# Optimization experiments

Hardware: AMD Instinct MI355X
Metric: run time of the kernel (lower is better)

The kernel has to match this reference:

```python
import jax, jax.numpy as jnp
import numpy as np

N_NODES = 20000   # num_of_nodes + 1 (incl. prediction node)
FEAT = 256        # in_features == hidden_features == out_features
N_LAYERS = 2
ALPHA = 0.2       # LeakyReLU negative slope
V_OBS = 512       # observed codes per patient
D_H = np.sqrt(FEAT * 1.0)  # sqrt(hidden_features * num_of_heads), n_heads=1
EPS = 1e-6


def _fc_edges(nodes):
    # torch: source = nodes.repeat(1, n); dest = each node repeated n times
    n = len(nodes)
    return np.stack([np.tile(nodes, n), np.repeat(nodes, n)]).astype(np.int64)


def setup_inputs() -> dict:
    key = jax.random.key(0)
    ks = jax.random.split(key, 16)
    rng = np.random.default_rng(0)
    obs = np.sort(rng.choice(np.arange(1, N_NODES - 1), size=V_OBS, replace=False))
    input_edges = jnp.asarray(_fc_edges(obs))
    obs_out = np.concatenate([obs, [N_NODES - 1]])  # add prediction node
    output_edges = jnp.asarray(_fc_edges(obs_out))

    s = 0.02
    embed = s * jax.random.normal(ks[0], (N_NODES, FEAT), jnp.float32)
    embed = embed.at[0].set(0.0)  # padding_idx=0
    return {
        "embed": embed,
        "W_w": s * jax.random.normal(ks[1], (N_LAYERS, FEAT, FEAT), jnp.float32),
        "W_b": s * jax.random.normal(ks[2], (N_LAYERS, FEAT), jnp.float32),
        "a": s * jax.random.normal(ks[3], (N_LAYERS, 2 * FEAT), jnp.float32),
        "ln_a": jnp.ones((N_LAYERS, FEAT), jnp.float32),
        "ln_b": jnp.zeros((N_LAYERS, FEAT), jnp.float32),
        "Wo_w": s * jax.random.normal(ks[4], (FEAT, FEAT), jnp.float32),
        "Wo_b": s * jax.random.normal(ks[5], (FEAT,), jnp.float32),
        "ao": s * jax.random.normal(ks[6], (2 * FEAT,), jnp.float32),
        "lno_a": jnp.ones((FEAT,), jnp.float32),
        "lno_b": jnp.zeros((FEAT,), jnp.float32),
        "lin_w": s * jax.random.normal(ks[7], (FEAT, FEAT), jnp.float32),
        "lin_b": s * jax.random.normal(ks[8], (FEAT,), jnp.float32),
        "param_w": s * jax.random.normal(ks[9], (2 * FEAT, FEAT), jnp.float32),
        "param_b": s * jax.random.normal(ks[10], (2 * FEAT,), jnp.float32),
        "out1_w": s * jax.random.normal(ks[11], (FEAT, FEAT), jnp.float32),
        "out1_b": s * jax.random.normal(ks[12], (FEAT,), jnp.float32),
        "out2_w": s * jax.random.normal(ks[13], (1, FEAT), jnp.float32),
        "out2_b": s * jax.random.normal(ks[14], (1,), jnp.float32),
        "input_edges": input_edges,
        "output_edges": output_edges,
    }


def _attention(x, edges, Ww, Wb, avec):
    # d = Linear(x): (N, H)
    d = x @ Ww.T + Wb
    H = d.shape[1]
    # a . [d_src ; d_dst] == (d @ a_left)[src] + (d @ a_right)[dst]  (cheaper, same math)
    s_node = d @ avec[:H]
    t_node = d @ avec[H:]
    score = s_node[edges[0]] + t_node[edges[1]]                  # (E,)
    e = jnp.exp(jax.nn.leaky_relu(score, ALPHA) / D_H)           # unnormalized attn
    n = x.shape[0]
    rowsum = jax.ops.segment_sum(e, edges[0], num_segments=n)   # (N,)
    agg = jax.ops.segment_sum(e[:, None] * d[edges[1]], edges[0], num_segments=n)
    zero = rowsum == 0
    # rows with no in-edges get an identity self-edge of weight 1 and rowsum 1
    agg = agg + jnp.where(zero[:, None], d, 0.0)
    return agg / jnp.where(zero, 1.0, rowsum)[:, None]


def _layernorm(x, g, b):
    m = x.mean(-1, keepdims=True)
    s = jnp.std(x, axis=-1, ddof=1, keepdims=True)  # torch std: unbiased
    return g * (x - m) / (s + EPS) + b


def reference(embed, W_w, W_b, a, ln_a, ln_b, Wo_w, Wo_b, ao, lno_a, lno_b,
              lin_w, lin_b, param_w, param_b, out1_w, out1_b, out2_w, out2_b,
              input_edges, output_edges):
    h = embed  # embedding lookup of arange(N) == the full table
    for l in range(N_LAYERS):  # in_att stack, concat=True, n_heads=1: ffn = LN -> ELU
        h = jax.nn.elu(_layernorm(_attention(h, input_edges, W_w[l], W_b[l], a[l]),
                                  ln_a[l], ln_b[l]))
    # variational layer (eval mode: reparameterize returns mu)
    hp = (h @ param_w.T + param_b).reshape(-1, 2, FEAT)
    h = hp[:, 0, :]  # mu
    # out_att: concat=False, mean over 1 head; ffn = LN -> ReLU -> Linear
    g = _attention(h, output_edges, Wo_w, Wo_b, ao)
    g = jax.nn.relu(_layernorm(g, lno_a, lno_b)) @ lin_w.T + lin_b
    # out_layer on prediction node: ReLU -> Linear -> ReLU -> Linear(->1)
    z = jax.nn.relu(g[-1])
    z = jax.nn.relu(z @ out1_w.T + out1_b)
    logit = z @ out2_w.T + out2_b  # (1,)
    return logit
```

## Files before the change

kernel.cpp:

```cpp
#include <hip/hip_runtime.h>
#include <hip/hip_bf16.h>

#define FEAT 256
#define NOBS 512
#define NOUT 513
#define GAT_ALPHA 0.2f
#define INV_DH (1.0f / 16.0f)
#define LN_EPS 1e-6f


__device__ __forceinline__ float b2f(unsigned short u) {
    union { float f; unsigned v; } x;
    x.v = ((unsigned)u) << 16;
    return x.f;
}

__device__ __forceinline__ float loadv(const void* p, long idx, int isbf) {
    if (isbf) return b2f(((const unsigned short*)p)[idx]);
    return ((const float*)p)[idx];
}

__device__ __forceinline__ float4 load4(const void* p, long idx, int isbf) {
    if (isbf) {
        ushort4 u = *(const ushort4*)((const unsigned short*)p + idx);
        return make_float4(b2f(u.x), b2f(u.y), b2f(u.z), b2f(u.w));
    }
    return *(const float4*)((const float*)p + idx);
}

__device__ __forceinline__ int detect_bf(const void* w) {
    const unsigned short* hb = (const unsigned short*)w;
    int sane = 0;
#pragma unroll
    for (int i = 0; i < 32; i += 2) {
        float a = fabsf(b2f(hb[i]));
        sane += (a > 1e-4f && a < 0.3f) ? 1 : 0;
    }
    return (sane >= 8) ? 1 : 0;
}

__device__ __forceinline__ int detect_estep(const void* edges) {
    const int* ei = (const int*)edges;
    return (ei[1] == 0 && ei[3] == 0 && ei[5] == 0 && ei[7] == 0) ? 2 : 1;
}

__device__ __forceinline__ float wave_allreduce(float v) {
#pragma unroll
    for (int o = 1; o < 64; o <<= 1) v += __shfl_xor(v, o);
    return v;
}

__device__ __forceinline__ float bsum1024(float v, float* red) {
    __syncthreads();
    float s = wave_allreduce(v);
    int lane = threadIdx.x & 63, w = threadIdx.x >> 6;
    if (lane == 0) red[w] = s;
    __syncthreads();
    float t = 0.f;
#pragma unroll
    for (int i = 0; i < 16; i++) t += red[i];
    return t;
}

#define FV_AS0 0
#define FV_AS1 256
#define FV_AT0 512
#define FV_AT1 768
#define FV_WB0 1024
#define FV_WB1 1280
#define FV_LNA0 1536
#define FV_LNA1 1792
#define FV_LNB0 2048
#define FV_LNB1 2304
#define FV_WOB 2560
#define FV_AOS 2816
#define FV_AOT 3072
#define FV_LNOA 3328
#define FV_LNOB 3584
#define FV_LINB 3840
#define FV_PARB 4096
#define FV_O1B 4352
#define FV_O2W 4608
#define FV_O2B 4864

__global__ __launch_bounds__(256) void k_front(
        const void* embed, const void* W_w, const void* W_b, const void* a,
        const void* ln_a, const void* ln_b, const void* Wo_w, const void* Wo_b,
        const void* ao, const void* lno_a, const void* lno_b, const void* lin_w,
        const void* lin_b, const void* param_w, const void* param_b,
        const void* out1_w, const void* out1_b, const void* out2_w, const void* out2_b,
        const void* oedges, float* fv, float* packs,
        float* __restrict__ D1, float* S1, float* T1, int* done) {
    __shared__ __align__(16) char smem[37888];
    float (*xs)[FEAT] = (float(*)[FEAT])smem;
    float (*wl)[33] = (float(*)[33])(smem + 4096);
    float (*tile)[65] = (float(*)[65])smem;
    int isbf = detect_bf(W_w);
    int b = blockIdx.x, tid = threadIdx.x, lane = tid & 63, w = tid >> 6;
    if (b < 129) {
        int estep = detect_estep(oedges);
        int i0 = b << 2;
        int nr = NOUT - i0;
        if (nr > 4) nr = 4;
        if (w < nr) {
            const int* oe = (const int*)oedges;
            long node = oe[(long)(i0 + w) * estep];
            *(float4*)&xs[w][lane << 2] = load4(embed, node * FEAT + (lane << 2), isbf);
        } else {
#pragma unroll
            for (int q = 0; q < 4; q++) xs[w][(lane << 2) + q] = 0.f;
        }
        float acc[4] = {0.f, 0.f, 0.f, 0.f};
        int fb8 = tid >> 3;
        int kq = tid & 7;
        for (int kc = 0; kc < 8; kc++) {
            int k0 = kc << 5;
            __syncthreads();
#pragma unroll
            for (int i = 0; i < 8; i++) {
                int f = fb8 + (i << 5);
                float4 v = load4(W_w, (long)f * FEAT + k0 + (kq << 2), isbf);
                wl[f][(kq << 2) + 0] = v.x;
                wl[f][(kq << 2) + 1] = v.y;
                wl[f][(kq << 2) + 2] = v.z;
                wl[f][(kq << 2) + 3] = v.w;
            }
            __syncthreads();
#pragma unroll
            for (int k4 = 0; k4 < 8; k4++) {
                float4 x0 = ((const float4*)xs[0])[(kc << 3) + k4];
                float4 x1 = ((const float4*)xs[1])[(kc << 3) + k4];
                float4 x2 = ((const float4*)xs[2])[(kc << 3) + k4];
                float4 x3 = ((const float4*)xs[3])[(kc << 3) + k4];
                float xa0[4] = {x0.x, x0.y, x0.z, x0.w};
                float xa1[4] = {x1.x, x1.y, x1.z, x1.w};
                float xa2[4] = {x2.x, x2.y, x2.z, x2.w};
                float xa3[4] = {x3.x, x3.y, x3.z, x3.w};
#pragma unroll
                for (int j = 0; j < 4; j++) {
                    float wv = wl[tid][(k4 << 2) + j];
                    acc[0] += xa0[j] * wv;
                    acc[1] += xa1[j] * wv;
                    acc[2] += xa2[j] * wv;
                    acc[3] += xa3[j] * wv;
                }
            }
        }
        float bb = loadv(W_b, tid, isbf);
#pragma unroll
        for (int j = 0; j < 4; j++) acc[j] += bb;
#pragma unroll
        for (int j = 0; j < 4; j++)
            if (j < nr) D1[(long)(i0 + j) * FEAT + tid] = acc[j];
        __syncthreads();
#pragma unroll
        for (int j = 0; j < 4; j++) xs[j][tid] = acc[j];
        __syncthreads();
        if (w < nr) {
            float sv = 0.f, tv = 0.f;
#pragma unroll
            for (int q = 0; q < 4; q++) {
                int f = lane + (q << 6);
                float dv = xs[w][f];
                sv += dv * loadv(a, f, isbf);
                tv += dv * loadv(a, FEAT + f, isbf);
            }
            sv = wave_allreduce(sv);
            tv = wave_allreduce(tv);
            if (lane == 0) { S1[i0 + w] = sv; T1[i0 + w] = tv; }
        }
    } else if (b < 209) {
        int job = b - 129;
        int m = 1 + (job >> 4), t = job & 15;
        int f0 = (t >> 2) << 6, k0 = (t & 3) << 6;
        const void* base;
        long eoff = 0;
        switch (m) {
            case 1: base = W_w; eoff = 65536; break;
            case 2: base = param_w; break;
            case 3: base = Wo_w; break;
            case 4: base = lin_w; break;
            default: base = out1_w; break;
        }
        int r = tid >> 2, cq = (tid & 3) << 4;
#pragma unroll
        for (int jj = 0; jj < 4; jj++) {
            float4 v = load4(base, eoff + (long)(f0 + r) * FEAT + k0 + cq + (jj << 2), isbf);
            tile[r][cq + (jj << 2) + 0] = v.x;
            tile[r][cq + (jj << 2) + 1] = v.y;
            tile[r][cq + (jj << 2) + 2] = v.z;
            tile[r][cq + (jj << 2) + 3] = v.w;
        }
        __syncthreads();
        float4* pack = (float4*)(packs + (long)m * 65536);
#pragma unroll
        for (int it = 0; it < 4; it++) {
            int kk = ((w << 2) + it) << 2;
            float4 v = make_float4(tile[lane][kk], tile[lane][kk + 1],
                                   tile[lane][kk + 2], tile[lane][kk + 3]);
            int k4g = (k0 >> 2) + (w << 2) + it;
            pack[(k4g << 8) + f0 + lane] = v;
        }
    } else {
        int cid = b - 209;
        const void* s;
        long so = 0;
        float* d;
        int n = 256;
        switch (cid) {
            case 0:  s = a;       so = 0;   d = fv + FV_AS0;  break;
            case 1:  s = a;       so = 512; d = fv + FV_AS1;  break;
            case 2:  s = a;       so = 256; d = fv + FV_AT0;  break;
            case 3:  s = a;       so = 768; d = fv + FV_AT1;  break;
            case 4:  s = W_b;     so = 0;   d = fv + FV_WB0;  break;
            case 5:  s = W_b;     so = 256; d = fv + FV_WB1;  break;
            case 6:  s = ln_a;    so = 0;   d = fv + FV_LNA0; break;
            case 7:  s = ln_a;    so = 256; d = fv + FV_LNA1; break;
            case 8:  s = ln_b;    so = 0;   d = fv + FV_LNB0; break;
            case 9:  s = ln_b;    so = 256; d = fv + FV_LNB1; break;
            case 10: s = Wo_b;    so = 0;   d = fv + FV_WOB;  break;
            case 11: s = ao;      so = 0;   d = fv + FV_AOS;  break;
            case 12: s = ao;      so = 256; d = fv + FV_AOT;  break;
            case 13: s = lno_a;   so = 0;   d = fv + FV_LNOA; break;
            case 14: s = lno_b;   so = 0;   d = fv + FV_LNOB; break;
            case 15: s = lin_b;   so = 0;   d = fv + FV_LINB; break;
            case 16: s = param_b; so = 0;   d = fv + FV_PARB; break;
            case 17: s = out1_b;  so = 0;   d = fv + FV_O1B;  break;
            case 18: s = out2_w;  so = 0;   d = fv + FV_O2W;  break;
            default: s = out2_b;  so = 0;   d = fv + FV_O2B;  n = 1; break;
        }
        for (int idx = tid; idx < n; idx += FEAT) d[idx] = loadv(s, so + idx, isbf);
        if (cid == 19 && tid == 0)
            __hip_atomic_store(done, 0, __ATOMIC_RELAXED, __HIP_MEMORY_SCOPE_AGENT);
    }
}

__device__ void tail_head(const float* __restrict__ D, const float* __restrict__ S,
                          const float* __restrict__ T, const float* __restrict__ fv,
                          const float4* __restrict__ PL, const float4* __restrict__ PO1,
                          int isbf, void* out, float* e, float (*wacc)[FEAT],
                          float (*part)[FEAT], float* ys, float* zs, float* red) {
    int tid = threadIdx.x, lane = tid & 63, w = tid >> 6;
    float sN = S[NOUT - 1];
    float p = 0.f;
    if (tid < NOUT) {
        float sc = sN + T[tid];
        sc = (sc > 0.f ? sc : GAT_ALPHA * sc) * INV_DH;
        float ev = __expf(sc);
        e[tid] = ev;
        p = ev;
    }
    float rowsum = bsum1024(p, red);
    float4 a4 = make_float4(0.f, 0.f, 0.f, 0.f);
    for (int j = w; j < NOUT; j += 16) {
        float ej = e[j];
        float4 dv = *(const float4*)(D + (long)j * FEAT + (lane << 2));
        a4.x += ej * dv.x; a4.y += ej * dv.y;
        a4.z += ej * dv.z; a4.w += ej * dv.w;
    }
    *(float4*)&wacc[w][lane << 2] = a4;
    __syncthreads();
    float val = 0.f;
    if (tid < FEAT) {
#pragma unroll
        for (int q = 0; q < 16; q++) val += wacc[q][tid];
        val /= rowsum;
    }
    float m = bsum1024(tid < FEAT ? val : 0.f, red) * (1.f / FEAT);
    float dv = (tid < FEAT) ? val - m : 0.f;
    float var = bsum1024(dv * dv, red) * (1.f / (FEAT - 1));
    if (tid < FEAT) {
        float y = fv[FV_LNOA + tid] * dv / (sqrtf(var) + LN_EPS) + fv[FV_LNOB + tid];
        ys[tid] = fmaxf(y, 0.f);
    }
    __syncthreads();
    int f = tid & 255, kq = tid >> 8;
    float g = 0.f;
#pragma unroll
    for (int q = 0; q < 16; q++) {
        int k4 = (kq << 4) + q;
        float4 wv = PL[(k4 << 8) + f];
        float4 yv = ((const float4*)ys)[k4];
        g += yv.x * wv.x + yv.y * wv.y + yv.z * wv.z + yv.w * wv.w;
    }
    part[kq][f] = g;
    __syncthreads();
    if (tid < FEAT) {
        float gg = part[0][tid] + part[1][tid] + part[2][tid] + part[3][tid] + fv[FV_LINB + tid];
        zs[tid] = fmaxf(gg, 0.f);
    }
    __syncthreads();
    float g2 = 0.f;
#pragma unroll
    for (int q = 0; q < 16; q++) {
        int k4 = (kq << 4) + q;
        float4 wv = PO1[(k4 << 8) + f];
        float4 zv = ((const float4*)zs)[k4];
        g2 += zv.x * wv.x + zv.y * wv.y + zv.z * wv.z + zv.w * wv.w;
    }
    __syncthreads();
    part[kq][f] = g2;
    __syncthreads();
    float z2 = 0.f;
    if (tid < FEAT) {
        z2 = part[0][tid] + part[1][tid] + part[2][tid] + part[3][tid] + fv[FV_O1B + tid];
        z2 = fmaxf(z2, 0.f);
        z2 *= fv[FV_O2W + tid];
    }
    float logit = bsum1024(z2, red) + fv[FV_O2B];
    if (tid == 0) {
        if (isbf) ((__hip_bfloat16*)out)[0] = __float2bfloat16(logit);
        else ((float*)out)[0] = logit;
    }
}

template <bool PWO, bool TAIL>
__global__ __launch_bounds__(1024) void k_mid(
        const float* __restrict__ Din, const float* __restrict__ Sin,
        const float* __restrict__ Tin, const float* __restrict__ ga,
        const float* __restrict__ gb, const float4* __restrict__ W1,
        const float* __restrict__ b1, const float4* __restrict__ W2,
        const float* __restrict__ b2v, const float* __restrict__ as_,
        const float* __restrict__ at_, float* __restrict__ Dout,
        float* Sout, float* Tout,
        const float* fvFull, const float4* PL, const float4* PO1,
        const void* dtypeP, int* done, void* out) {
    __shared__ __align__(16) float e[2][NOBS];
    __shared__ __align__(16) float sacc[16][2][FEAT];
    __shared__ __align__(16) float xs[2][FEAT];
    __shared__ __align__(16) float part[4][2][FEAT];
    __shared__ float redA[16];
    __shared__ float redB[16];
    __shared__ float rsh[2];
    __shared__ int lastflag;
    int tid = threadIdx.x, lane = tid & 63, w = tid >> 6;
    int b = blockIdx.x;
    bool fb = (b == 256);
    int i0 = b << 1;
    int nr = fb ? 1 : 2;
    int row = (tid >> 8) & 1, f = tid & 255;

    float val = 0.f;
    if (!fb) {
        int rr = tid >> 9, j = tid & 511;
        float sc = Sin[i0 + rr] + Tin[j];
        sc = (sc > 0.f ? sc : GAT_ALPHA * sc) * INV_DH;
        e[rr][j] = __expf(sc);
        __syncthreads();
        int r2 = w >> 3, seg = w & 7;
        float pv = wave_allreduce(e[r2][(seg << 6) + lane]);
        if (lane == 0) redA[w] = pv;
        __syncthreads();
        if (tid < 2) {
            float s = 0.f;
#pragma unroll
            for (int q = 0; q < 8; q++) s += redA[(tid << 3) + q];
            rsh[tid] = s;
        }
        float4 a0 = make_float4(0.f, 0.f, 0.f, 0.f), a1 = a0;
        for (int j2 = w; j2 < NOBS; j2 += 16) {
            float4 dv = *(const float4*)(Din + (long)j2 * FEAT + (lane << 2));
            float e0 = e[0][j2], e1 = e[1][j2];
            a0.x += e0 * dv.x; a0.y += e0 * dv.y; a0.z += e0 * dv.z; a0.w += e0 * dv.w;
            a1.x += e1 * dv.x; a1.y += e1 * dv.y; a1.z += e1 * dv.z; a1.w += e1 * dv.w;
        }
        *(float4*)&sacc[w][0][lane << 2] = a0;
        *(float4*)&sacc[w][1][lane << 2] = a1;
        __syncthreads();
        if (tid < 512) {
#pragma unroll
            for (int q = 0; q < 16; q++) val += sacc[q][row][f];
            val /= rsh[row];
        }
    } else {
        if (tid < 512) val = (row == 0) ? Din[(long)NOBS * FEAT + f] : 0.f;
    }

    __syncthreads();
    float s1 = wave_allreduce(tid < 512 ? val : 0.f);
    if (lane == 0) redA[w] = s1;
    __syncthreads();
    float m = (redA[(row << 2)] + redA[(row << 2) + 1] +
               redA[(row << 2) + 2] + redA[(row << 2) + 3]) * (1.f / FEAT);
    float dvv = (tid < 512) ? val - m : 0.f;
    __syncthreads();
    float s2 = wave_allreduce(dvv * dvv);
    if (lane == 0) redA[w] = s2;
    __syncthreads();
    float var = (redA[(row << 2)] + redA[(row << 2) + 1] +
                 redA[(row << 2) + 2] + redA[(row << 2) + 3]) * (1.f / (FEAT - 1));
    if (tid < 512) {
        float isd = 1.f / (sqrtf(var) + LN_EPS);
        float y = ga[f] * dvv * isd + gb[f];
        xs[row][f] = (y > 0.f) ? y : (__expf(y) - 1.f);
    }
    __syncthreads();

    int q = tid >> 8;
    float ac0 = 0.f, ac1 = 0.f;
#pragma unroll
    for (int t = 0; t < 16; t++) {
        int k4 = (q << 4) + t;
        float4 wv = W1[(k4 << 8) + f];
        float4 x0 = ((const float4*)xs[0])[k4];
        float4 x1 = ((const float4*)xs[1])[k4];
        ac0 += x0.x * wv.x + x0.y * wv.y + x0.z * wv.z + x0.w * wv.w;
        ac1 += x1.x * wv.x + x1.y * wv.y + x1.z * wv.z + x1.w * wv.w;
    }
    part[q][0][f] = ac0;
    part[q][1][f] = ac1;
    __syncthreads();
    float dval = 0.f;
    if (tid < 512)
        dval = part[0][row][f] + part[1][row][f] + part[2][row][f] + part[3][row][f] + b1[f];
    if (PWO) {
        __syncthreads();
        if (tid < 512) xs[row][f] = dval;
        __syncthreads();
        float bc0 = 0.f, bc1 = 0.f;
#pragma unroll
        for (int t = 0; t < 16; t++) {
            int k4 = (q << 4) + t;
            float4 wv = W2[(k4 << 8) + f];
            float4 x0 = ((const float4*)xs[0])[k4];
            float4 x1 = ((const float4*)xs[1])[k4];
            bc0 += x0.x * wv.x + x0.y * wv.y + x0.z * wv.z + x0.w * wv.w;
            bc1 += x1.x * wv.x + x1.y * wv.y + x1.z * wv.z + x1.w * wv.w;
        }
        __syncthreads();
        part[q][0][f] = bc0;
        part[q][1][f] = bc1;
        __syncthreads();
        if (tid < 512)
            dval = part[0][row][f] + part[1][row][f] + part[2][row][f] + part[3][row][f] + b2v[f];
    }
    if (tid < 512 && row < nr)
        Dout[(long)(i0 + row) * FEAT + f] = dval;

    __syncthreads();
    float sv = wave_allreduce(tid < 512 ? dval * as_[f] : 0.f);
    float tv = wave_allreduce(tid < 512 ? dval * at_[f] : 0.f);
    if (lane == 0) { redA[w] = sv; redB[w] = tv; }
    __syncthreads();
    if (tid < nr) {
        float ss = redA[(tid << 2)] + redA[(tid << 2) + 1] +
                   redA[(tid << 2) + 2] + redA[(tid << 2) + 3];
        float tt = redB[(tid << 2)] + redB[(tid << 2) + 1] +
                   redB[(tid << 2) + 2] + redB[(tid << 2) + 3];
        Sout[i0 + tid] = ss;
        Tout[i0 + tid] = tt;
    }

    if (TAIL) {
        __syncthreads();
        if (tid == 0) {
            __threadfence();
            int old = atomicAdd(done, 1);
            lastflag = (old == 256) ? 1 : 0;
        }
        __syncthreads();
        if (lastflag) {
            if (tid == 0) __threadfence();
            __syncthreads();
            int isbf = detect_bf(dtypeP);
            tail_head(Dout, Sout, Tout, fvFull, PL, PO1, isbf, out,
                      (float*)e, (float(*)[FEAT])sacc, (float(*)[FEAT])part,
                      (float*)part + 4 * FEAT, (float*)part + 5 * FEAT, redA);
        }
    }
}

extern "C" void kernel_launch(void* const* d_in, const int* in_sizes, int n_in,
                              void* d_out, int out_size, void* d_ws, size_t ws_size,
                              hipStream_t stream) {
    const void* embed = d_in[0];
    const void* W_w = d_in[1];
    const void* W_b = d_in[2];
    const void* a = d_in[3];
    const void* ln_a = d_in[4];
    const void* ln_b = d_in[5];
    const void* Wo_w = d_in[6];
    const void* Wo_b = d_in[7];
    const void* ao = d_in[8];
    const void* lno_a = d_in[9];
    const void* lno_b = d_in[10];
    const void* lin_w = d_in[11];
    const void* lin_b = d_in[12];
    const void* param_w = d_in[13];
    const void* param_b = d_in[14];
    const void* out1_w = d_in[15];
    const void* out1_b = d_in[16];
    const void* out2_w = d_in[17];
    const void* out2_b = d_in[18];
    const void* oedges = d_in[20];

    char* ws = (char*)d_ws;
    int* done = (int*)ws;
    float* fv = (float*)(ws + 256);
    float* packs = (float*)(ws + 32768);
    float* D1 = (float*)(ws + 1605632);
    float* D2 = (float*)(ws + 2131200);
    float* S1 = (float*)(ws + 2656768);
    float* T1 = (float*)(ws + 2660864);
    float* S2 = (float*)(ws + 2664960);
    float* T2 = (float*)(ws + 2669056);

    const float4* P1 = (const float4*)(packs + 1 * 65536);
    const float4* PP = (const float4*)(packs + 2 * 65536);
    const float4* PWo = (const float4*)(packs + 3 * 65536);
    const float4* PL = (const float4*)(packs + 4 * 65536);
    const float4* PO1 = (const float4*)(packs + 5 * 65536);

    k_front<<<229, FEAT, 0, stream>>>(embed, W_w, W_b, a, ln_a, ln_b, Wo_w, Wo_b, ao,
                                      lno_a, lno_b, lin_w, lin_b, param_w, param_b,
                                      out1_w, out1_b, out2_w, out2_b, oedges,
                                      fv, packs, D1, S1, T1, done);
    k_mid<false, false><<<257, 1024, 0, stream>>>(D1, S1, T1, fv + FV_LNA0, fv + FV_LNB0,
                                                  P1, fv + FV_WB1, nullptr, nullptr,
                                                  fv + FV_AS1, fv + FV_AT1, D2, S2, T2,
                                                  nullptr, nullptr, nullptr, nullptr,
                                                  nullptr, nullptr);
    k_mid<true, true><<<257, 1024, 0, stream>>>(D2, S2, T2, fv + FV_LNA1, fv + FV_LNB1,
                                                PP, fv + FV_PARB, PWo, fv + FV_WOB,
                                                fv + FV_AOS, fv + FV_AOT, D1, S1, T1,
                                                fv, PL, PO1, W_w, done, d_out);
}
```

Baseline: 96.88 us.

## Process one row per block in mid kernels and split tail into separate kernel

The mid-layer kernels now handle one node row per 1024-thread block (513 blocks) instead of two rows per block (257 blocks). This doubles parallelism but also doubles the reads of weight tiles and D per row. The last-block atomic counter tail is replaced by a separate single-block tail kernel launch. That removes the atomic and fence work but adds a kernel launch boundary.

Result: slower. 99.66 us (+2.9%).

```diff
diff --git a/kernel.cpp b/kernel.cpp
--- a/kernel.cpp
+++ b/kernel.cpp
@@ -90,7 +90,7 @@
         const void* lin_b, const void* param_w, const void* param_b,
         const void* out1_w, const void* out1_b, const void* out2_w, const void* out2_b,
         const void* oedges, float* fv, float* packs,
-        float* __restrict__ D1, float* S1, float* T1, int* done) {
+        float* __restrict__ D1, float* S1, float* T1) {
     __shared__ __align__(16) char smem[37888];
     float (*xs)[FEAT] = (float(*)[FEAT])smem;
     float (*wl)[33] = (float(*)[33])(smem + 4096);
@@ -230,16 +230,117 @@
             default: s = out2_b;  so = 0;   d = fv + FV_O2B;  n = 1; break;
         }
         for (int idx = tid; idx < n; idx += FEAT) d[idx] = loadv(s, so + idx, isbf);
-        if (cid == 19 && tid == 0)
-            __hip_atomic_store(done, 0, __ATOMIC_RELAXED, __HIP_MEMORY_SCOPE_AGENT);
-    }
-}
-
-__device__ void tail_head(const float* __restrict__ D, const float* __restrict__ S,
-                          const float* __restrict__ T, const float* __restrict__ fv,
-                          const float4* __restrict__ PL, const float4* __restrict__ PO1,
-                          int isbf, void* out, float* e, float (*wacc)[FEAT],
-                          float (*part)[FEAT], float* ys, float* zs, float* red) {
+    }
+}
+
+template <bool PWO>
+__global__ __launch_bounds__(1024, 8) void k_mid(
+        const float* __restrict__ Din, const float* __restrict__ Sin,
+        const float* __restrict__ Tin, const float* __restrict__ ga,
+        const float* __restrict__ gb, const float4* __restrict__ W1,
+        const float* __restrict__ b1, const float4* __restrict__ W2,
+        const float* __restrict__ b2v, const float* __restrict__ as_,
+        const float* __restrict__ at_, float* __restrict__ Dout,
+        float* Sout, float* Tout) {
+    __shared__ __align__(16) float e[NOBS];
+    __shared__ __align__(16) float sacc[16][FEAT];
+    __shared__ __align__(16) float xs[FEAT];
+    __shared__ __align__(16) float part[4][FEAT];
+    __shared__ float red[16];
+    int tid = threadIdx.x, lane = tid & 63, w = tid >> 6;
+    int i = blockIdx.x;
+    bool fb = (i == NOBS);
+
+    float val = 0.f;
+    if (!fb) {
+        float si = Sin[i];
+        float p = 0.f;
+        if (tid < NOBS) {
+            float sc = si + Tin[tid];
+            sc = (sc > 0.f ? sc : GAT_ALPHA * sc) * INV_DH;
+            float ev = __expf(sc);
+            e[tid] = ev;
+            p = ev;
+        }
+        float rowsum = bsum1024(p, red);
+        float4 a4 = make_float4(0.f, 0.f, 0.f, 0.f);
+        for (int j = w; j < NOBS; j += 16) {
+            float ej = e[j];
+            float4 dv = *(const float4*)(Din + (long)j * FEAT + (lane << 2));
+            a4.x += ej * dv.x; a4.y += ej * dv.y;
+            a4.z += ej * dv.z; a4.w += ej * dv.w;
+        }
+        *(float4*)&sacc[w][lane << 2] = a4;
+        __syncthreads();
+        if (tid < FEAT) {
+#pragma unroll
+            for (int q = 0; q < 16; q++) val += sacc[q][tid];
+            val /= rowsum;
+        }
+    } else {
+        if (tid < FEAT) val = Din[(long)NOBS * FEAT + tid];
+    }
+
+    float m = bsum1024(tid < FEAT ? val : 0.f, red) * (1.f / FEAT);
+    float dvv = (tid < FEAT) ? val - m : 0.f;
+    float var = bsum1024(dvv * dvv, red) * (1.f / (FEAT - 1));
+    if (tid < FEAT) {
+        float y = ga[tid] * dvv / (sqrtf(var) + LN_EPS) + gb[tid];
+        xs[tid] = (y > 0.f) ? y : (__expf(y) - 1.f);
+    }
+    __syncthreads();
+
+    int q = tid >> 8, f = tid & 255;
+    float g = 0.f;
+#pragma unroll
+    for (int t = 0; t < 16; t++) {
+        int k4 = (q << 4) + t;
+        float4 wv = W1[(k4 << 8) + f];
+        float4 xv = ((const float4*)xs)[k4];
+        g += xv.x * wv.x + xv.y * wv.y + xv.z * wv.z + xv.w * wv.w;
+    }
+    part[q][f] = g;
+    __syncthreads();
+    float dval = 0.f;
+    if (tid < FEAT)
+        dval = part[0][tid] + part[1][tid] + part[2][tid] + part[3][tid] + b1[tid];
+    if (PWO) {
+        __syncthreads();
+        if (tid < FEAT) xs[tid] = dval;
+        __syncthreads();
+        float g2 = 0.f;
+#pragma unroll
+        for (int t = 0; t < 16; t++) {
+            int k4 = (q << 4) + t;
+            float4 wv = W2[(k4 << 8) + f];
+            float4 xv = ((const float4*)xs)[k4];
+            g2 += xv.x * wv.x + xv.y * wv.y + xv.z * wv.z + xv.w * wv.w;
+        }
+        __syncthreads();
+        part[q][f] = g2;
+        __syncthreads();
+        if (tid < FEAT)
+            dval = part[0][tid] + part[1][tid] + part[2][tid] + part[3][tid] + b2v[tid];
+    }
+    if (tid < FEAT) Dout[(long)i * FEAT + tid] = dval;
+
+    float sv = bsum1024(tid < FEAT ? dval * as_[tid] : 0.f, red);
+    float tv = bsum1024(tid < FEAT ? dval * at_[tid] : 0.f, red);
+    if (tid == 0) { Sout[i] = sv; Tout[i] = tv; }
+}
+
+__global__ __launch_bounds__(1024) void k_tail(
+        const float* __restrict__ D, const float* __restrict__ S,
+        const float* __restrict__ T, const float* __restrict__ fv,
+        const float4* __restrict__ PL, const float4* __restrict__ PO1,
+        const void* dtypeP, void* out) {
+    __shared__ __align__(16) float e[NOUT + 7];
+    __shared__ __align__(16) float wacc[16][FEAT];
+    __shared__ __align__(16) float part[4][FEAT];
+    __shared__ __align__(16) float ys[FEAT];
+    __shared__ __align__(16) float zs[FEAT];
+    __shared__ float red[16];
+    int isbf = detect_bf(dtypeP);
     int tid = threadIdx.x, lane = tid & 63, w = tid >> 6;
     float sN = S[NOUT - 1];
     float p = 0.f;
@@ -311,162 +412,6 @@
     if (tid == 0) {
         if (isbf) ((__hip_bfloat16*)out)[0] = __float2bfloat16(logit);
         else ((float*)out)[0] = logit;
-    }
-}
-
-template <bool PWO, bool TAIL>
-__global__ __launch_bounds__(1024) void k_mid(
-        const float* __restrict__ Din, const float* __restrict__ Sin,
-        const float* __restrict__ Tin, const float* __restrict__ ga,
-        const float* __restrict__ gb, const float4* __restrict__ W1,
-        const float* __restrict__ b1, const float4* __restrict__ W2,
-        const float* __restrict__ b2v, const float* __restrict__ as_,
-        const float* __restrict__ at_, float* __restrict__ Dout,
-        float* Sout, float* Tout,
-        const float* fvFull, const float4* PL, const float4* PO1,
-        const void* dtypeP, int* done, void* out) {
-    __shared__ __align__(16) float e[2][NOBS];
-    __shared__ __align__(16) float sacc[16][2][FEAT];
-    __shared__ __align__(16) float xs[2][FEAT];
-    __shared__ __align__(16) float part[4][2][FEAT];
-    __shared__ float redA[16];
-    __shared__ float redB[16];
-    __shared__ float rsh[2];
-    __shared__ int lastflag;
-    int tid = threadIdx.x, lane = tid & 63, w = tid >> 6;
-    int b = blockIdx.x;
-    bool fb = (b == 256);
-    int i0 = b << 1;
-    int nr = fb ? 1 : 2;
-    int row = (tid >> 8) & 1, f = tid & 255;
-
-    float val = 0.f;
-    if (!fb) {
-        int rr = tid >> 9, j = tid & 511;
-        float sc = Sin[i0 + rr] + Tin[j];
-        sc = (sc > 0.f ? sc : GAT_ALPHA * sc) * INV_DH;
-        e[rr][j] = __expf(sc);
-        __syncthreads();
-        int r2 = w >> 3, seg = w & 7;
-        float pv = wave_allreduce(e[r2][(seg << 6) + lane]);
-        if (lane == 0) redA[w] = pv;
-        __syncthreads();
-        if (tid < 2) {
-            float s = 0.f;
-#pragma unroll
-            for (int q = 0; q < 8; q++) s += redA[(tid << 3) + q];
-            rsh[tid] = s;
-        }
-        float4 a0 = make_float4(0.f, 0.f, 0.f, 0.f), a1 = a0;
-        for (int j2 = w; j2 < NOBS; j2 += 16) {
-            float4 dv = *(const float4*)(Din + (long)j2 * FEAT + (lane << 2));
-            float e0 = e[0][j2], e1 = e[1][j2];
-            a0.x += e0 * dv.x; a0.y += e0 * dv.y; a0.z += e0 * dv.z; a0.w += e0 * dv.w;
-            a1.x += e1 * dv.x; a1.y += e1 * dv.y; a1.z += e1 * dv.z; a1.w += e1 * dv.w;
-        }
-        *(float4*)&sacc[w][0][lane << 2] = a0;
-        *(float4*)&sacc[w][1][lane << 2] = a1;
-        __syncthreads();
-        if (tid < 512) {
-#pragma unroll
-            for (int q = 0; q < 16; q++) val += sacc[q][row][f];
-            val /= rsh[row];
-        }
-    } else {
-        if (tid < 512) val = (row == 0) ? Din[(long)NOBS * FEAT + f] : 0.f;
-    }
-
-    __syncthreads();
-    float s1 = wave_allreduce(tid < 512 ? val : 0.f);
-    if (lane == 0) redA[w] = s1;
-    __syncthreads();
-    float m = (redA[(row << 2)] + redA[(row << 2) + 1] +
-               redA[(row << 2) + 2] + redA[(row << 2) + 3]) * (1.f / FEAT);
-    float dvv = (tid < 512) ? val - m : 0.f;
-    __syncthreads();
-    float s2 = wave_allreduce(dvv * dvv);
-    if (lane == 0) redA[w] = s2;
-    __syncthreads();
-    float var = (redA[(row << 2)] + redA[(row << 2) + 1] +
-                 redA[(row << 2) + 2] + redA[(row << 2) + 3]) * (1.f / (FEAT - 1));
-    if (tid < 512) {
-        float isd = 1.f / (sqrtf(var) + LN_EPS);
-        float y = ga[f] * dvv * isd + gb[f];
-        xs[row][f] = (y > 0.f) ? y : (__expf(y) - 1.f);
-    }
-    __syncthreads();
-
-    int q = tid >> 8;
-    float ac0 = 0.f, ac1 = 0.f;
-#pragma unroll
-    for (int t = 0; t < 16; t++) {
-        int k4 = (q << 4) + t;
-        float4 wv = W1[(k4 << 8) + f];
-        float4 x0 = ((const float4*)xs[0])[k4];
-        float4 x1 = ((const float4*)xs[1])[k4];
-        ac0 += x0.x * wv.x + x0.y * wv.y + x0.z * wv.z + x0.w * wv.w;
-        ac1 += x1.x * wv.x + x1.y * wv.y + x1.z * wv.z + x1.w * wv.w;
-    }
-    part[q][0][f] = ac0;
-    part[q][1][f] = ac1;
-    __syncthreads();
-    float dval = 0.f;
-    if (tid < 512)
-        dval = part[0][row][f] + part[1][row][f] + part[2][row][f] + part[3][row][f] + b1[f];
-    if (PWO) {
-        __syncthreads();
-        if (tid < 512) xs[row][f] = dval;
-        __syncthreads();
-        float bc0 = 0.f, bc1 = 0.f;
-#pragma unroll
-        for (int t = 0; t < 16; t++) {
-            int k4 = (q << 4) + t;
-            float4 wv = W2[(k4 << 8) + f];
-            float4 x0 = ((const float4*)xs[0])[k4];
-            float4 x1 = ((const float4*)xs[1])[k4];
-            bc0 += x0.x * wv.x + x0.y * wv.y + x0.z * wv.z + x0.w * wv.w;
-            bc1 += x1.x * wv.x + x1.y * wv.y + x1.z * wv.z + x1.w * wv.w;
-        }
-        __syncthreads();
-        part[q][0][f] = bc0;
-        part[q][1][f] = bc1;
-        __syncthreads();
-        if (tid < 512)
-            dval = part[0][row][f] + part[1][row][f] + part[2][row][f] + part[3][row][f] + b2v[f];
-    }
-    if (tid < 512 && row < nr)
-        Dout[(long)(i0 + row) * FEAT + f] = dval;
-
-    __syncthreads();
-    float sv = wave_allreduce(tid < 512 ? dval * as_[f] : 0.f);
-    float tv = wave_allreduce(tid < 512 ? dval * at_[f] : 0.f);
-    if (lane == 0) { redA[w] = sv; redB[w] = tv; }
-    __syncthreads();
-    if (tid < nr) {
-        float ss = redA[(tid << 2)] + redA[(tid << 2) + 1] +
-                   redA[(tid << 2) + 2] + redA[(tid << 2) + 3];
-        float tt = redB[(tid << 2)] + redB[(tid << 2) + 1] +
-                   redB[(tid << 2) + 2] + redB[(tid << 2) + 3];
-        Sout[i0 + tid] = ss;
-        Tout[i0 + tid] = tt;
-    }
-
-    if (TAIL) {
-        __syncthreads();
-        if (tid == 0) {
-            __threadfence();
-            int old = atomicAdd(done, 1);
-            lastflag = (old == 256) ? 1 : 0;
-        }
-        __syncthreads();
-        if (lastflag) {
-            if (tid == 0) __threadfence();
-            __syncthreads();
-            int isbf = detect_bf(dtypeP);
-            tail_head(Dout, Sout, Tout, fvFull, PL, PO1, isbf, out,
-                      (float*)e, (float(*)[FEAT])sacc, (float(*)[FEAT])part,
-                      (float*)part + 4 * FEAT, (float*)part + 5 * FEAT, redA);
-        }
     }
 }
 
@@ -495,7 +440,6 @@
     const void* oedges = d_in[20];
 
     char* ws = (char*)d_ws;
-    int* done = (int*)ws;
     float* fv = (float*)(ws + 256);
     float* packs = (float*)(ws + 32768);
     float* D1 = (float*)(ws + 1605632);
@@ -514,14 +458,12 @@
     k_front<<<229, FEAT, 0, stream>>>(embed, W_w, W_b, a, ln_a, ln_b, Wo_w, Wo_b, ao,
                                       lno_a, lno_b, lin_w, lin_b, param_w, param_b,
                                       out1_w, out1_b, out2_w, out2_b, oedges,
-                                      fv, packs, D1, S1, T1, done);
-    k_mid<false, false><<<257, 1024, 0, stream>>>(D1, S1, T1, fv + FV_LNA0, fv + FV_LNB0,
-                                                  P1, fv + FV_WB1, nullptr, nullptr,
-                                                  fv + FV_AS1, fv + FV_AT1, D2, S2, T2,
-                                                  nullptr, nullptr, nullptr, nullptr,
-                                                  nullptr, nullptr);
-    k_mid<true, true><<<257, 1024, 0, stream>>>(D2, S2, T2, fv + FV_LNA1, fv + FV_LNB1,
-                                                PP, fv + FV_PARB, PWo, fv + FV_WOB,
-                                                fv + FV_AOS, fv + FV_AOT, D1, S1, T1,
-                                                fv, PL, PO1, W_w, done, d_out);
-}
+                                      fv, packs, D1, S1, T1);
+    k_mid<false><<<NOUT, 1024, 0, stream>>>(D1, S1, T1, fv + FV_LNA0, fv + FV_LNB0,
+                                            P1, fv + FV_WB1, nullptr, nullptr,
+                                            fv + FV_AS1, fv + FV_AT1, D2, S2, T2);
+    k_mid<true><<<NOUT, 1024, 0, stream>>>(D2, S2, T2, fv + FV_LNA1, fv + FV_LNB1,
+                                           PP, fv + FV_PARB, PWo, fv + FV_WOB,
+                                           fv + FV_AOS, fv + FV_AOT, D1, S1, T1);
+    k_tail<<<1, 1024, 0, stream>>>(D1, S1, T1, fv, PL, PO1, W_w, d_out);
+}
```
